# Optimization experiments

Hardware: AMD Instinct MI355X
Metric: run time of the kernel (lower is better)

Reference implementation:

```python
import jax, jax.numpy as jnp
import numpy as np

D_Z, D_Y, N, N_SAMPLE = 512, 32, 2048, 128
JITTER = 0.0001


def setup_inputs() -> dict:
    key = jax.random.key(0)
    k1, k2, k3, k4, k5 = jax.random.split(key, 5)
    d_total = D_Z + N * D_Y
    return {
        "m": jax.random.normal(k1, (d_total,), jnp.float32),
        "Lz": jax.random.normal(k2, (D_Z, D_Z), jnp.float32),
        "Ly_blocks": jax.random.normal(k3, (N, D_Y, D_Y), jnp.float32),
        "Lyz": jax.random.normal(k4, (N * D_Y, D_Z), jnp.float32),
        "eps": jax.random.normal(k5, (N_SAMPLE, d_total), jnp.float32),
    }


def reference(m, Lz, Ly_blocks, Lyz, eps):
    # L_dense (block lower-triangular) is never materialized; we compute
    # z = m + eps @ L_dense.T block-wise. L_dense = [[tril(Lz), 0], [Lyz, blkdiag(tril(Ly_n))]] + jitter*I.
    dt = Lz.dtype
    Lz_t = jnp.tril(Lz) + JITTER * jnp.eye(D_Z, dtype=dt)
    Ly = jnp.tril(Ly_blocks) + JITTER * jnp.eye(D_Y, dtype=dt)  # [N, d_y, d_y]

    eps_z = eps[:, :D_Z]                          # [S, d_z]
    eps_y = eps[:, D_Z:].reshape(-1, N, D_Y)      # [S, N, d_y]

    z_z = m[:D_Z] + eps_z @ Lz_t.T                # [S, d_z]
    cross = eps_z @ Lyz.T                         # [S, N*d_y]
    diag = jnp.einsum("snj,nij->sni", eps_y, Ly).reshape(-1, N * D_Y)
    z_y = m[D_Z:] + cross + diag                  # [S, N*d_y]
    return jnp.concatenate([z_z, z_y], axis=1)
```

## Files before the change

### kernel.cpp

```cpp
#include <hip/hip_runtime.h>

#define DZ 512
#define DT 66048
#define NT 4128
#define SV_JITTER 1e-4f

typedef __attribute__((ext_vector_type(8))) short bf8;
typedef __attribute__((ext_vector_type(4))) float f4;

__device__ __forceinline__ short f2bf(float f) {
  unsigned u = __builtin_bit_cast(unsigned, f);
  return (short)((u + 0x7FFFu + ((u >> 16) & 1u)) >> 16);
}

__device__ __forceinline__ bf8 cvt8(float4 a, float4 b) {
  bf8 r = { f2bf(a.x), f2bf(a.y), f2bf(a.z), f2bf(a.w),
            f2bf(b.x), f2bf(b.y), f2bf(b.z), f2bf(b.w) };
  return r;
}

__device__ __forceinline__ bf8 cvt8_tril(float4 x, float4 y, int kbase, int diag) {
  float v[8] = {x.x, x.y, x.z, x.w, y.x, y.y, y.z, y.w};
  bf8 r;
  #pragma unroll
  for (int t = 0; t < 8; ++t) {
    int k = kbase + t;
    float val = (k < diag) ? v[t] : ((k == diag) ? v[t] + SV_JITTER : 0.f);
    r[t] = f2bf(val);
  }
  return r;
}

template <bool IS_Z>
__device__ __forceinline__ void process_tile(
    int col0, int lcol, int q, int lane, const short* __restrict__ Afrag,
    const float* __restrict__ mv, const float* __restrict__ Lz,
    const float* __restrict__ Ly, const float* __restrict__ Lyz,
    const float* __restrict__ eps, float* __restrict__ out) {
  const int colL = col0 + lcol;
  const float* bptr = IS_Z ? (Lz + (size_t)colL * DZ)
                           : (Lyz + (size_t)(colL - DZ) * DZ);
  const int bdiag = colL;

  f4 acc[8];
  #pragma unroll
  for (int mi = 0; mi < 8; ++mi) acc[mi] = f4{0.f, 0.f, 0.f, 0.f};

  float4 bx0, by0, bx1, by1, bx2, by2, bx3, by3;
  bf8 a0[8], a1[8];

  auto loadB = [&](int kk, float4& x, float4& y) {
    const float* p = bptr + kk * 32 + 8 * q;
    x = *(const float4*)p;
    y = *(const float4*)(p + 4);
  };
  auto loadA = [&](int kk, bf8* a) {
    #pragma unroll
    for (int mi = 0; mi < 8; ++mi)
      a[mi] = *(const bf8*)&Afrag[(kk * 8 + mi) * 512 + lane * 8];
  };
  auto mk = [&](float4 x, float4 y, int kb) {
    return IS_Z ? cvt8_tril(x, y, kb, bdiag) : cvt8(x, y);
  };
  auto domfma = [&](const bf8* a, bf8 bf) {
    #pragma unroll
    for (int mi = 0; mi < 8; ++mi)
      acc[mi] = __builtin_amdgcn_mfma_f32_16x16x32_bf16(a[mi], bf, acc[mi], 0, 0, 0);
  };

  loadB(0, bx0, by0); loadB(1, bx1, by1);
  loadB(2, bx2, by2); loadB(3, bx3, by3);
  loadA(0, a0); loadA(1, a1);

  int kk = 0;
  #pragma unroll 1
  for (int kt = 0; kt < 3; ++kt, kk += 4) {
    { bf8 bf = mk(bx0, by0, kk * 32 + 8 * q);
      domfma(a0, bf); loadB(kk + 4, bx0, by0); loadA(kk + 2, a0); }
    { bf8 bf = mk(bx1, by1, (kk + 1) * 32 + 8 * q);
      domfma(a1, bf); loadB(kk + 5, bx1, by1); loadA(kk + 3, a1); }
    { bf8 bf = mk(bx2, by2, (kk + 2) * 32 + 8 * q);
      domfma(a0, bf); loadB(kk + 6, bx2, by2); loadA(kk + 4, a0); }
    { bf8 bf = mk(bx3, by3, (kk + 3) * 32 + 8 * q);
      domfma(a1, bf); loadB(kk + 7, bx3, by3); loadA(kk + 5, a1); }
  }

  float4 dbx{}, dby{};
  int nb = 0, dI = 0;
  if (!IS_Z) {
    nb = (col0 - DZ) >> 5;
    dI = (col0 - DZ) & 31;
    const float* pb = Ly + ((size_t)nb * 32 + dI + lcol) * 32 + 8 * q;
    dbx = *(const float4*)pb; dby = *(const float4*)(pb + 4);
  }

  { bf8 bf = mk(bx0, by0, 12 * 32 + 8 * q); domfma(a0, bf); loadA(14, a0); }
  { bf8 bf = mk(bx1, by1, 13 * 32 + 8 * q); domfma(a1, bf); loadA(15, a1); }
  { bf8 bf = mk(bx2, by2, 14 * 32 + 8 * q); domfma(a0, bf); }
  { bf8 bf = mk(bx3, by3, 15 * 32 + 8 * q); domfma(a1, bf); }

  if (!IS_Z) {
    const bf8 dbf = cvt8_tril(dbx, dby, 8 * q, dI + lcol);
    const float* abase = eps + (size_t)lcol * DT + DZ + nb * 32 + 8 * q;
    float4 rx[4], ry[4];
    #pragma unroll
    for (int mi = 0; mi < 4; ++mi) {
      const float* pa = abase + (size_t)mi * 16 * DT;
      rx[mi] = *(const float4*)pa; ry[mi] = *(const float4*)(pa + 4);
    }
    float4 sx[4], sy[4];
    #pragma unroll
    for (int mi = 0; mi < 4; ++mi) {
      const float* pa = abase + (size_t)(mi + 4) * 16 * DT;
      sx[mi] = *(const float4*)pa; sy[mi] = *(const float4*)(pa + 4);
    }
    #pragma unroll
    for (int mi = 0; mi < 4; ++mi) {
      bf8 af = cvt8(rx[mi], ry[mi]);
      acc[mi] = __builtin_amdgcn_mfma_f32_16x16x32_bf16(af, dbf, acc[mi], 0, 0, 0);
    }
    #pragma unroll
    for (int mi = 0; mi < 4; ++mi) {
      bf8 af = cvt8(sx[mi], sy[mi]);
      acc[mi + 4] = __builtin_amdgcn_mfma_f32_16x16x32_bf16(af, dbf, acc[mi + 4], 0, 0, 0);
    }
  }

  const float mval = mv[colL];
  #pragma unroll
  for (int mi = 0; mi < 8; ++mi) {
    #pragma unroll
    for (int r = 0; r < 4; ++r) {
      out[(size_t)(16 * mi + 4 * q + r) * DT + colL] = acc[mi][r] + mval;
    }
  }
}

__global__ __launch_bounds__(512, 2)
void sv_kernel(const float* __restrict__ mv, const float* __restrict__ Lz,
               const float* __restrict__ Ly, const float* __restrict__ Lyz,
               const float* __restrict__ eps, float* __restrict__ out) {
  __shared__ short Afrag[128 * 512];

  const int tid = threadIdx.x;
  const int lane = tid & 63;
  const int wv = tid >> 6;
  const int lcol = lane & 15;
  const int q = lane >> 4;

  {
    const int slot = tid & 63;
    const int r0 = (tid >> 6) * 16;
    #pragma unroll 4
    for (int i = 0; i < 16; ++i) {
      const int r = r0 + i;
      const float* p = eps + (size_t)(16 * (r & 7) + (slot & 15)) * DT +
                       (r >> 3) * 32 + (slot >> 4) * 8;
      float4 x = *(const float4*)p;
      float4 y = *(const float4*)(p + 4);
      *(bf8*)&Afrag[r * 512 + slot * 8] = cvt8(x, y);
    }
  }
  __syncthreads();

  #pragma unroll 1
  for (int r = 0; r < 3; ++r) {
    const int T = r * 2048 + blockIdx.x * 8 + wv;
    if (T >= NT) break;
    const int col0 = T * 16;
    if (col0 < DZ)
      process_tile<true>(col0, lcol, q, lane, Afrag, mv, Lz, Ly, Lyz, eps, out);
    else
      process_tile<false>(col0, lcol, q, lane, Afrag, mv, Lz, Ly, Lyz, eps, out);
  }
}

extern "C" void kernel_launch(void* const* d_in, const int* in_sizes, int n_in,
                              void* d_out, int out_size, void* d_ws, size_t ws_size,
                              hipStream_t stream) {
  const float* m   = (const float*)d_in[0];
  const float* Lz  = (const float*)d_in[1];
  const float* Ly  = (const float*)d_in[2];
  const float* Lyz = (const float*)d_in[3];
  const float* eps = (const float*)d_in[4];
  float* out = (float*)d_out;
  sv_kernel<<<dim3(256), dim3(512), 0, stream>>>(m, Lz, Ly, Lyz, eps, out);
}
```

Baseline: 55.12 us.

## Double waves per block so each wave handles one tile, shrinking register use

```diff
diff --git a/kernel.cpp b/kernel.cpp
--- a/kernel.cpp
+++ b/kernel.cpp
@@ -47,14 +47,14 @@
   for (int mi = 0; mi < 8; ++mi) acc[mi] = f4{0.f, 0.f, 0.f, 0.f};
 
   float4 bx0, by0, bx1, by1, bx2, by2, bx3, by3;
-  bf8 a0[8], a1[8];
+  bf8 a[8];
 
   auto loadB = [&](int kk, float4& x, float4& y) {
     const float* p = bptr + kk * 32 + 8 * q;
     x = *(const float4*)p;
     y = *(const float4*)(p + 4);
   };
-  auto loadA = [&](int kk, bf8* a) {
+  auto loadA = [&](int kk) {
     #pragma unroll
     for (int mi = 0; mi < 8; ++mi)
       a[mi] = *(const bf8*)&Afrag[(kk * 8 + mi) * 512 + lane * 8];
@@ -62,7 +62,7 @@
   auto mk = [&](float4 x, float4 y, int kb) {
     return IS_Z ? cvt8_tril(x, y, kb, bdiag) : cvt8(x, y);
   };
-  auto domfma = [&](const bf8* a, bf8 bf) {
+  auto domfma = [&](bf8 bf) {
     #pragma unroll
     for (int mi = 0; mi < 8; ++mi)
       acc[mi] = __builtin_amdgcn_mfma_f32_16x16x32_bf16(a[mi], bf, acc[mi], 0, 0, 0);
@@ -70,19 +70,22 @@
 
   loadB(0, bx0, by0); loadB(1, bx1, by1);
   loadB(2, bx2, by2); loadB(3, bx3, by3);
-  loadA(0, a0); loadA(1, a1);
 
   int kk = 0;
   #pragma unroll 1
   for (int kt = 0; kt < 3; ++kt, kk += 4) {
-    { bf8 bf = mk(bx0, by0, kk * 32 + 8 * q);
-      domfma(a0, bf); loadB(kk + 4, bx0, by0); loadA(kk + 2, a0); }
-    { bf8 bf = mk(bx1, by1, (kk + 1) * 32 + 8 * q);
-      domfma(a1, bf); loadB(kk + 5, bx1, by1); loadA(kk + 3, a1); }
-    { bf8 bf = mk(bx2, by2, (kk + 2) * 32 + 8 * q);
-      domfma(a0, bf); loadB(kk + 6, bx2, by2); loadA(kk + 4, a0); }
-    { bf8 bf = mk(bx3, by3, (kk + 3) * 32 + 8 * q);
-      domfma(a1, bf); loadB(kk + 7, bx3, by3); loadA(kk + 5, a1); }
+    { loadA(kk);
+      bf8 bf = mk(bx0, by0, kk * 32 + 8 * q);
+      loadB(kk + 4, bx0, by0); domfma(bf); }
+    { loadA(kk + 1);
+      bf8 bf = mk(bx1, by1, (kk + 1) * 32 + 8 * q);
+      loadB(kk + 5, bx1, by1); domfma(bf); }
+    { loadA(kk + 2);
+      bf8 bf = mk(bx2, by2, (kk + 2) * 32 + 8 * q);
+      loadB(kk + 6, bx2, by2); domfma(bf); }
+    { loadA(kk + 3);
+      bf8 bf = mk(bx3, by3, (kk + 3) * 32 + 8 * q);
+      loadB(kk + 7, bx3, by3); domfma(bf); }
   }
 
   float4 dbx{}, dby{};
@@ -94,10 +97,10 @@
     dbx = *(const float4*)pb; dby = *(const float4*)(pb + 4);
   }
 
-  { bf8 bf = mk(bx0, by0, 12 * 32 + 8 * q); domfma(a0, bf); loadA(14, a0); }
-  { bf8 bf = mk(bx1, by1, 13 * 32 + 8 * q); domfma(a1, bf); loadA(15, a1); }
-  { bf8 bf = mk(bx2, by2, 14 * 32 + 8 * q); domfma(a0, bf); }
-  { bf8 bf = mk(bx3, by3, 15 * 32 + 8 * q); domfma(a1, bf); }
+  { loadA(12); bf8 bf = mk(bx0, by0, 12 * 32 + 8 * q); domfma(bf); }
+  { loadA(13); bf8 bf = mk(bx1, by1, 13 * 32 + 8 * q); domfma(bf); }
+  { loadA(14); bf8 bf = mk(bx2, by2, 14 * 32 + 8 * q); domfma(bf); }
+  { loadA(15); bf8 bf = mk(bx3, by3, 15 * 32 + 8 * q); domfma(bf); }
 
   if (!IS_Z) {
     const bf8 dbf = cvt8_tril(dbx, dby, 8 * q, dI + lcol);
@@ -108,12 +111,6 @@
       const float* pa = abase + (size_t)mi * 16 * DT;
       rx[mi] = *(const float4*)pa; ry[mi] = *(const float4*)(pa + 4);
     }
-    float4 sx[4], sy[4];
-    #pragma unroll
-    for (int mi = 0; mi < 4; ++mi) {
-      const float* pa = abase + (size_t)(mi + 4) * 16 * DT;
-      sx[mi] = *(const float4*)pa; sy[mi] = *(const float4*)(pa + 4);
-    }
     #pragma unroll
     for (int mi = 0; mi < 4; ++mi) {
       bf8 af = cvt8(rx[mi], ry[mi]);
@@ -121,7 +118,12 @@
     }
     #pragma unroll
     for (int mi = 0; mi < 4; ++mi) {
-      bf8 af = cvt8(sx[mi], sy[mi]);
+      const float* pa = abase + (size_t)(mi + 4) * 16 * DT;
+      rx[mi] = *(const float4*)pa; ry[mi] = *(const float4*)(pa + 4);
+    }
+    #pragma unroll
+    for (int mi = 0; mi < 4; ++mi) {
+      bf8 af = cvt8(rx[mi], ry[mi]);
       acc[mi + 4] = __builtin_amdgcn_mfma_f32_16x16x32_bf16(af, dbf, acc[mi + 4], 0, 0, 0);
     }
   }
@@ -136,7 +138,7 @@
   }
 }
 
-__global__ __launch_bounds__(512, 2)
+__global__ __launch_bounds__(1024, 4)
 void sv_kernel(const float* __restrict__ mv, const float* __restrict__ Lz,
                const float* __restrict__ Ly, const float* __restrict__ Lyz,
                const float* __restrict__ eps, float* __restrict__ out) {
@@ -149,10 +151,10 @@
   const int q = lane >> 4;
 
   {
-    const int slot = tid & 63;
-    const int r0 = (tid >> 6) * 16;
+    const int slot = lane;
+    const int r0 = wv * 8;
     #pragma unroll 4
-    for (int i = 0; i < 16; ++i) {
+    for (int i = 0; i < 8; ++i) {
       const int r = r0 + i;
       const float* p = eps + (size_t)(16 * (r & 7) + (slot & 15)) * DT +
                        (r >> 3) * 32 + (slot >> 4) * 8;
@@ -163,15 +165,17 @@
   }
   __syncthreads();
 
-  #pragma unroll 1
-  for (int r = 0; r < 3; ++r) {
-    const int T = r * 2048 + blockIdx.x * 8 + wv;
-    if (T >= NT) break;
+  {
+    const int T = blockIdx.x * 16 + wv;
     const int col0 = T * 16;
     if (col0 < DZ)
       process_tile<true>(col0, lcol, q, lane, Afrag, mv, Lz, Ly, Lyz, eps, out);
     else
       process_tile<false>(col0, lcol, q, lane, Afrag, mv, Lz, Ly, Lyz, eps, out);
+  }
+  if (wv == 15 && blockIdx.x < 32) {
+    const int col0 = (4096 + blockIdx.x) * 16;
+    process_tile<false>(col0, lcol, q, lane, Afrag, mv, Lz, Ly, Lyz, eps, out);
   }
 }
 
@@ -184,5 +188,5 @@
   const float* Lyz = (const float*)d_in[3];
   const float* eps = (const float*)d_in[4];
   float* out = (float*)d_out;
-  sv_kernel<<<dim3(256), dim3(512), 0, stream>>>(m, Lz, Ly, Lyz, eps, out);
+  sv_kernel<<<dim3(256), dim3(1024), 0, stream>>>(m, Lz, Ly, Lyz, eps, out);
 }
```

Measured after the change: 51.28 us. 1.07x faster.
